# Kernel tuning notes

Measured on AMD Instinct MI355X. Metric: run time of the kernel, lower is better.

## Reference

```python
import jax, jax.numpy as jnp
import numpy as np

N = 50000   # num_nodes
T = 8       # num_time_steps
C = 64      # feature width (num_features == hidden == num_classes == 64, forced by the module's shape constraints)
E = 800000  # num_edges


def temporal_conv(x, edge_index, time_index, W, b, perturb=None):
    """Faithful TemporalAGNNConv.forward: per-timestep masked scatter-add of
    neighbor features, concat over T, linear + relu. Implemented as a single
    fused (t, dst)-bucketed segment reduce instead of T separate propagates.
    Note: self.lin is dead code in the original; self-loop addition in the
    original would crash (time_index length mismatch) so edges are used as-is.
    """
    src, dst = edge_index[0], edge_index[1]
    msgs = x[src]                                   # [E, C] gather
    seg = time_index * N + dst                      # combined (t, node) bucket
    agg = jax.ops.segment_sum(msgs, seg, num_segments=T * N)   # [T*N, C]
    cat = agg.reshape(T, N, C).transpose(1, 0, 2).reshape(N, T * C)  # [N, T*C]
    out = jax.nn.relu(cat @ W + b)                  # temporal_lin + relu
    if perturb is not None:
        out = out + perturb
    return out


def setup_inputs() -> dict:
    key = jax.random.key(0)
    ks = jax.random.split(key, 11)
    x = jax.random.normal(ks[0], (N, C), jnp.float32)
    edge_index = jax.random.randint(ks[1], (2, E), 0, N, dtype=jnp.int32)
    time_index = jax.random.randint(ks[2], (E,), 0, T, dtype=jnp.int32)
    s_t = 1.0 / np.sqrt(T * C).astype(np.float32)
    # temporal_lin weights stored as [in, out] (torch Linear transposed)
    Wt1 = jax.random.uniform(ks[3], (T * C, C), jnp.float32, -s_t, s_t)
    bt1 = jax.random.uniform(ks[4], (C,), jnp.float32, -s_t, s_t)
    Wt2 = jax.random.uniform(ks[5], (T * C, C), jnp.float32, -s_t, s_t)
    bt2 = jax.random.uniform(ks[6], (C,), jnp.float32, -s_t, s_t)
    s_a1 = 1.0 / np.sqrt(C).astype(np.float32)
    Wa1 = jax.random.uniform(ks[7], (C, 128), jnp.float32, -s_a1, s_a1)
    ba1 = jax.random.uniform(ks[8], (128,), jnp.float32, -s_a1, s_a1)
    s_a2 = 1.0 / np.sqrt(128).astype(np.float32)
    Wa2 = jax.random.uniform(ks[9], (128, C), jnp.float32, -s_a2, s_a2)
    ba2 = jax.random.uniform(ks[10], (C,), jnp.float32, -s_a2, s_a2)
    return {"x": x, "edge_index": edge_index, "time_index": time_index,
            "Wt1": Wt1, "bt1": bt1, "Wt2": Wt2, "bt2": bt2,
            "Wa1": Wa1, "ba1": ba1, "Wa2": Wa2, "ba2": ba2}


def reference(x, edge_index, time_index, Wt1, bt1, Wt2, bt2, Wa1, ba1, Wa2, ba2):
    h1 = jax.nn.relu(temporal_conv(x, edge_index, time_index, Wt1, bt1))   # conv1 + relu
    h2 = temporal_conv(h1, edge_index, time_index, Wt2, bt2)               # conv2 (output width C)
    adv = jax.nn.relu(h2 @ Wa1 + ba1) @ Wa2 + ba2                          # adversary MLP -> [N, C]
    out = temporal_conv(x, edge_index, time_index, Wt1, bt1, perturb=adv)  # conv1 again + perturbation
    return out
```

## Files before the change

### kernel.cpp

```cpp
#include <hip/hip_runtime.h>

#define N_NODES 50000
#define C_FEAT  64
#define E_EDGES 800000
#define KEYS    400000
#define NBLK1   391
#define DPB     16
#define NTILES  (N_NODES / DPB)
#define PBLK_X  1563
#define PBLK_W  128
#define PBLK_A  64
#define PBLK_H  391
#define DPART   6250
#define CONV_GRID 1024

typedef __attribute__((ext_vector_type(8))) short short8;
typedef __attribute__((ext_vector_type(4))) float f32x4;

__device__ __forceinline__ float bf2f(unsigned short u) {
    union { unsigned int i; float f; } v; v.i = ((unsigned int)u) << 16; return v.f;
}
__device__ __forceinline__ unsigned short f2bf(float f) {
    union { float f; unsigned int i; } v; v.f = f;
    unsigned int r = v.i + 0x7fff + ((v.i >> 16) & 1);
    return (unsigned short)(r >> 16);
}

__global__ __launch_bounds__(256) void prep_hist(const float* __restrict__ x,
                                                 const float* __restrict__ W1,
                                                 const float* __restrict__ W2,
                                                 const float* __restrict__ Wa1,
                                                 const float* __restrict__ Wa2,
                                                 const int* __restrict__ dst,
                                                 const int* __restrict__ tix,
                                                 unsigned short* __restrict__ xb,
                                                 unsigned short* __restrict__ WT1,
                                                 unsigned short* __restrict__ WT2,
                                                 unsigned short* __restrict__ Wa1T,
                                                 unsigned short* __restrict__ Wa2T,
                                                 int* __restrict__ cnt) {
    const int b = blockIdx.x;
    if (b < PBLK_X) {
        int base = (b * 256 + threadIdx.x) * 8;
        if (base < N_NODES * 64) {
            float4 a = *(const float4*)(x + base);
            float4 c = *(const float4*)(x + base + 4);
            short8 o;
            o[0] = (short)f2bf(a.x); o[1] = (short)f2bf(a.y);
            o[2] = (short)f2bf(a.z); o[3] = (short)f2bf(a.w);
            o[4] = (short)f2bf(c.x); o[5] = (short)f2bf(c.y);
            o[6] = (short)f2bf(c.z); o[7] = (short)f2bf(c.w);
            *(short8*)(xb + base) = o;
        }
    } else if (b < PBLK_X + PBLK_W) {
        int i = (b - PBLK_X) * 256 + threadIdx.x;
        int n = i >> 9, k = i & 511;
        WT1[i] = f2bf(W1[k * 64 + n]);
        WT2[i] = f2bf(W2[k * 64 + n]);
    } else if (b < PBLK_X + PBLK_W + PBLK_A) {
        int i = (b - PBLK_X - PBLK_W) * 256 + threadIdx.x;
        if (i < 8192) {
            int n = i >> 6, k = i & 63;
            Wa1T[i] = f2bf(Wa1[k * 128 + n]);
        } else {
            int ii = i - 8192;
            int n = ii >> 7, k = ii & 127;
            Wa2T[ii] = f2bf(Wa2[k * 64 + n]);
        }
    } else {
        int bb = b - PBLK_X - PBLK_W - PBLK_A;
        const int e0 = bb * 2048 + threadIdx.x * 8;
        if (e0 < E_EDGES) {
            int4 d0 = *(const int4*)(dst + e0);
            int4 d1 = *(const int4*)(dst + e0 + 4);
            int4 t0 = *(const int4*)(tix + e0);
            int4 t1 = *(const int4*)(tix + e0 + 4);
            int dd[8] = {d0.x, d0.y, d0.z, d0.w, d1.x, d1.y, d1.z, d1.w};
            int tt[8] = {t0.x, t0.y, t0.z, t0.w, t1.x, t1.y, t1.z, t1.w};
            #pragma unroll
            for (int k = 0; k < 8; ++k)
                atomicAdd(&cnt[dd[k] * 8 + tt[k]], 1);
        }
    }
}

__global__ __launch_bounds__(256) void scan_all(int* __restrict__ cnt,
                                                int* __restrict__ bsum,
                                                int* __restrict__ chunkoff,
                                                int* __restrict__ done) {
    __shared__ int wsum[4];
    __shared__ int ticket;
    const int tid = threadIdx.x;
    const int lane = tid & 63;
    const int wave = tid >> 6;
    const int i4 = blockIdx.x * 256 + tid;
    int4 v = make_int4(0, 0, 0, 0);
    const bool ok = (i4 * 4 < KEYS);
    if (ok) v = ((const int4*)cnt)[i4];
    int s = v.x + v.y + v.z + v.w;
    int sc = s;
    #pragma unroll
    for (int d = 1; d < 64; d <<= 1) {
        int o = __shfl_up(sc, d, 64);
        if (lane >= d) sc += o;
    }
    if (lane == 63) wsum[wave] = sc;
    __syncthreads();
    int wbase = 0;
    #pragma unroll
    for (int w = 0; w < 4; ++w) wbase += (w < wave) ? wsum[w] : 0;
    int base = wbase + sc - s;
    int4 o;
    o.x = base;
    o.y = base + v.x;
    o.z = o.y + v.y;
    o.w = o.z + v.z;
    if (ok) ((int4*)cnt)[i4] = o;
    if (tid == 255) {
        bsum[blockIdx.x] = wbase + sc;
        __threadfence();
        ticket = atomicAdd(done, 1);
    }
    __syncthreads();
    if (ticket == NBLK1 - 1 && wave == 0) {
        int carry = 0;
        #pragma unroll
        for (int g = 0; g < (NBLK1 + 63) / 64; ++g) {
            int j = g * 64 + lane;
            int val = (j < NBLK1) ? atomicAdd(&bsum[j], 0) : 0;
            int scn = val;
            #pragma unroll
            for (int d = 1; d < 64; d <<= 1) {
                int oo = __shfl_up(scn, d, 64);
                if (lane >= d) scn += oo;
            }
            if (j < NBLK1) chunkoff[j] = carry + scn - val;
            carry += __shfl(scn, 63, 64);
        }
    }
}

__global__ __launch_bounds__(256) void scatter_edges(const int* __restrict__ src,
                                                     const int* __restrict__ dst,
                                                     const int* __restrict__ tix,
                                                     int* __restrict__ cursor,
                                                     const int* __restrict__ chunkoff,
                                                     int* __restrict__ elist) {
    const int g = blockIdx.x & 7;
    const int lo = g * DPART;
    const int e0 = (blockIdx.x >> 3) * 2048 + threadIdx.x * 8;
    if (e0 < E_EDGES) {
        int4 d0 = *(const int4*)(dst + e0);
        int4 d1 = *(const int4*)(dst + e0 + 4);
        int4 t0 = *(const int4*)(tix + e0);
        int4 t1 = *(const int4*)(tix + e0 + 4);
        int4 s0 = *(const int4*)(src + e0);
        int4 s1 = *(const int4*)(src + e0 + 4);
        int dd[8] = {d0.x, d0.y, d0.z, d0.w, d1.x, d1.y, d1.z, d1.w};
        int tt[8] = {t0.x, t0.y, t0.z, t0.w, t1.x, t1.y, t1.z, t1.w};
        int ss[8] = {s0.x, s0.y, s0.z, s0.w, s1.x, s1.y, s1.z, s1.w};
        #pragma unroll
        for (int k = 0; k < 8; ++k) {
            if ((unsigned)(dd[k] - lo) < (unsigned)DPART) {
                int key = dd[k] * 8 + tt[k];
                int pos = chunkoff[key >> 10] + atomicAdd(&cursor[key], 1);
                elist[pos] = ss[k] | (tt[k] << 16) | ((dd[k] & 15) << 19);
            }
        }
    }
}

#define FLUSH(P, V)                                                                   \
    { int _k = (P) >> 16;                                                             \
      if (_k != cur) { scat[cur >> 3][(cur & 7) * 64 + c] = f2bf(acc);                \
                       acc = 0.f; cur = _k; }                                         \
      acc += (V); }

#define EDGE(K)                                                                       \
    int p##K = __builtin_amdgcn_readlane(pv, e + K);                                  \
    float v##K = bf2f(Xb[(size_t)(p##K & 0xffff) * 64 + c]);

template <bool ADV>
__global__ __launch_bounds__(512, 8) void fused_conv(const unsigned short* __restrict__ Xb,
                                                     const unsigned short* __restrict__ WT,
                                                     const float* __restrict__ bias,
                                                     const int* __restrict__ segend,
                                                     const int* __restrict__ chunkoff,
                                                     const int* __restrict__ elist,
                                                     unsigned short* __restrict__ Hb,
                                                     const unsigned short* __restrict__ Wa1T,
                                                     const float* __restrict__ ba1,
                                                     const unsigned short* __restrict__ Wa2T,
                                                     const float* __restrict__ ba2,
                                                     const unsigned short* __restrict__ h1r,
                                                     float* __restrict__ outF) {
    __shared__ __attribute__((aligned(16))) unsigned short scat[DPB][520];
    unsigned short (*sH)[72]  = (unsigned short(*)[72])&scat[0][0];
    unsigned short (*sT)[136] = (unsigned short(*)[136])((char*)scat + 4096);
    const int lane = threadIdx.x & 63;
    const int wave = threadIdx.x >> 6;
    const int c = lane;

    for (int tile = blockIdx.x; tile < NTILES; tile += CONV_GRID) {
        const int dbase = tile * DPB;

        {
            short8 z = {};
            *(short8*)&scat[wave * 2 + 0][lane * 8] = z;
            *(short8*)&scat[wave * 2 + 1][lane * 8] = z;
        }

        const int dpair = dbase + wave * 2;
        const int k0 = dpair * 8;
        const int sbeg = (dpair == 0) ? 0 : chunkoff[(k0 - 1) >> 10] + segend[k0 - 1];
        const int send = chunkoff[(k0 + 15) >> 10] + segend[k0 + 15];
        int pv = (lane < send - sbeg) ? elist[sbeg + lane] : 0;

        {
            int i = sbeg;
            int cur = 0;
            float acc = 0.f;
            if (i < send) cur = __builtin_amdgcn_readlane(pv, 0) >> 16;
            while (i < send) {
                int cnt = send - i; cnt = (cnt > 64) ? 64 : cnt;
                int pvn = 0;
                if (i + 64 < send) pvn = (lane < send - i - 64) ? elist[i + 64 + lane] : 0;
                int e = 0;
                for (; e + 15 < cnt; e += 16) {
                    EDGE(0)  EDGE(1)  EDGE(2)  EDGE(3)
                    EDGE(4)  EDGE(5)  EDGE(6)  EDGE(7)
                    EDGE(8)  EDGE(9)  EDGE(10) EDGE(11)
                    EDGE(12) EDGE(13) EDGE(14) EDGE(15)
                    FLUSH(p0, v0)   FLUSH(p1, v1)   FLUSH(p2, v2)   FLUSH(p3, v3)
                    FLUSH(p4, v4)   FLUSH(p5, v5)   FLUSH(p6, v6)   FLUSH(p7, v7)
                    FLUSH(p8, v8)   FLUSH(p9, v9)   FLUSH(p10, v10) FLUSH(p11, v11)
                    FLUSH(p12, v12) FLUSH(p13, v13) FLUSH(p14, v14) FLUSH(p15, v15)
                }
                if (e + 7 < cnt) {
                    EDGE(0) EDGE(1) EDGE(2) EDGE(3) EDGE(4) EDGE(5) EDGE(6) EDGE(7)
                    FLUSH(p0, v0) FLUSH(p1, v1) FLUSH(p2, v2) FLUSH(p3, v3)
                    FLUSH(p4, v4) FLUSH(p5, v5) FLUSH(p6, v6) FLUSH(p7, v7)
                    e += 8;
                }
                if (e + 3 < cnt) {
                    EDGE(0) EDGE(1) EDGE(2) EDGE(3)
                    FLUSH(p0, v0) FLUSH(p1, v1) FLUSH(p2, v2) FLUSH(p3, v3)
                    e += 4;
                }
                if (e + 1 < cnt) {
                    EDGE(0) EDGE(1)
                    FLUSH(p0, v0) FLUSH(p1, v1)
                    e += 2;
                }
                if (e < cnt) {
                    EDGE(0)
                    FLUSH(p0, v0)
                }
                i += 64;
                pv = pvn;
            }
            if (sbeg < send)
                scat[cur >> 3][(cur & 7) * 64 + c] = f2bf(acc);
        }
        __syncthreads();

        const int m = lane & 15;
        const int quad = lane >> 4;
        f32x4 acc4 = {0.f, 0.f, 0.f, 0.f};
        if (wave < 4) {
            const int n0 = wave * 16;
            const unsigned short* wrow = WT + (size_t)(n0 + m) * 512;
            #pragma unroll
            for (int kc = 0; kc < 16; ++kc) {
                short8 af = *(const short8*)&scat[m][kc * 32 + quad * 8];
                short8 bf = *(const short8*)(wrow + kc * 32 + quad * 8);
                acc4 = __builtin_amdgcn_mfma_f32_16x16x32_bf16(af, bf, acc4, 0, 0, 0);
            }
        }

        if (!ADV) {
            if (wave < 4) {
                const int col = wave * 16 + m;
                const float bcol = bias[col];
                #pragma unroll
                for (int r = 0; r < 4; ++r) {
                    int node = dbase + quad * 4 + r;
                    Hb[(size_t)node * 64 + col] = f2bf(fmaxf(acc4[r] + bcol, 0.f));
                }
            }
        } else {
            __syncthreads();
            if (wave < 4) {
                const int col = wave * 16 + m;
                const float bcol = bias[col];
                #pragma unroll
                for (int r = 0; r < 4; ++r)
                    sH[quad * 4 + r][col] = f2bf(fmaxf(acc4[r] + bcol, 0.f));
            }
            __syncthreads();
            {
                f32x4 a1 = {0.f, 0.f, 0.f, 0.f};
                const int col = wave * 16 + m;
                #pragma unroll
                for (int kc = 0; kc < 2; ++kc) {
                    short8 af = *(const short8*)&sH[m][kc * 32 + quad * 8];
                    short8 bf = *(const short8*)(Wa1T + (size_t)col * 64 + kc * 32 + quad * 8);
                    a1 = __builtin_amdgcn_mfma_f32_16x16x32_bf16(af, bf, a1, 0, 0, 0);
                }
                const float b1 = ba1[col];
                #pragma unroll
                for (int r = 0; r < 4; ++r)
                    sT[quad * 4 + r][col] = f2bf(fmaxf(a1[r] + b1, 0.f));
            }
            __syncthreads();
            if (wave < 4) {
                f32x4 a2 = {0.f, 0.f, 0.f, 0.f};
                const int col = wave * 16 + m;
                #pragma unroll
                for (int kc = 0; kc < 4; ++kc) {
                    short8 af = *(const short8*)&sT[m][kc * 32 + quad * 8];
                    short8 bf = *(const short8*)(Wa2T + (size_t)col * 128 + kc * 32 + quad * 8);
                    a2 = __builtin_amdgcn_mfma_f32_16x16x32_bf16(af, bf, a2, 0, 0, 0);
                }
                const float b2 = ba2[col];
                #pragma unroll
                for (int r = 0; r < 4; ++r) {
                    int node = dbase + quad * 4 + r;
                    outF[(size_t)node * 64 + col] =
                        a2[r] + b2 + bf2f(h1r[(size_t)node * 64 + col]);
                }
            }
        }
        __syncthreads();
    }
}

extern "C" void kernel_launch(void* const* d_in, const int* in_sizes, int n_in,
                              void* d_out, int out_size, void* d_ws, size_t ws_size,
                              hipStream_t stream) {
    const float* x   = (const float*)d_in[0];
    const int*   ei  = (const int*)d_in[1];
    const int*   tix = (const int*)d_in[2];
    const float* Wt1 = (const float*)d_in[3];
    const float* bt1 = (const float*)d_in[4];
    const float* Wt2 = (const float*)d_in[5];
    const float* bt2 = (const float*)d_in[6];
    const float* Wa1 = (const float*)d_in[7];
    const float* ba1 = (const float*)d_in[8];
    const float* Wa2 = (const float*)d_in[9];
    const float* ba2 = (const float*)d_in[10];
    float* out = (float*)d_out;

    const int* src = ei;
    const int* dst = ei + E_EDGES;

    unsigned short* xb   = (unsigned short*)d_ws;
    unsigned short* h1b  = xb + (size_t)N_NODES * 64;
    unsigned short* h2b  = h1b + (size_t)N_NODES * 64;
    unsigned short* WT1  = h2b + (size_t)N_NODES * 64;
    unsigned short* WT2  = WT1 + 64 * 512;
    unsigned short* Wa1T = WT2 + 64 * 512;
    unsigned short* Wa2T = Wa1T + 8192;
    int* cnt      = (int*)(Wa2T + 8192);
    int* bsum     = cnt + KEYS;
    int* chunkoff = bsum + 512;
    int* done     = chunkoff + 512;
    int* elist    = done + 64;

    hipMemsetAsync(cnt, 0, (KEYS + 512 + 512 + 64) * sizeof(int), stream);
    prep_hist<<<PBLK_X + PBLK_W + PBLK_A + PBLK_H, 256, 0, stream>>>(
        x, Wt1, Wt2, Wa1, Wa2, dst, tix, xb, WT1, WT2, Wa1T, Wa2T, cnt);
    scan_all<<<NBLK1, 256, 0, stream>>>(cnt, bsum, chunkoff, done);
    scatter_edges<<<8 * 391, 256, 0, stream>>>(src, dst, tix, cnt, chunkoff, elist);

    fused_conv<false><<<CONV_GRID, 512, 0, stream>>>(
        xb, WT1, bt1, cnt, chunkoff, elist, h1b,
        nullptr, nullptr, nullptr, nullptr, nullptr, nullptr);
    fused_conv<true><<<CONV_GRID, 512, 0, stream>>>(
        h1b, WT2, bt2, cnt, chunkoff, elist, nullptr,
        Wa1T, ba1, Wa2T, ba2, h1b, out);
}
```

Before: 274.6 us.

## Balance edge work across waves with fp32 LDS accumulation and boundary atomics

Instead of each wave handling the edges of a fixed pair of destination nodes, the tile's whole edge range is split evenly across the 8 waves. Partial sums that cross wave boundaries are merged with LDS float atomics on each wave's first and last segment. The scatter buffer becomes fp32 and is converted to bf16 when the MFMA operands are loaded. This is meant to remove load imbalance from skewed per-node degrees, at the cost of a doubled LDS footprint, an extra barrier and per-kc conversion work.

```diff
diff --git a/kernel.cpp b/kernel.cpp
--- a/kernel.cpp
+++ b/kernel.cpp
@@ -13,6 +13,7 @@
 #define PBLK_H  391
 #define DPART   6250
 #define CONV_GRID 1024
+#define RS      516
 
 typedef __attribute__((ext_vector_type(8))) short short8;
 typedef __attribute__((ext_vector_type(4))) float f32x4;
@@ -172,8 +173,10 @@
 
 #define FLUSH(P, V)                                                                   \
     { int _k = (P) >> 16;                                                             \
-      if (_k != cur) { scat[cur >> 3][(cur & 7) * 64 + c] = f2bf(acc);                \
-                       acc = 0.f; cur = _k; }                                         \
+      if (_k != cur) {                                                               \
+          float* sp = scatf + (cur >> 3) * RS + (cur & 7) * 64 + c;                   \
+          if (first) { atomicAdd(sp, acc); first = false; } else *sp = acc;           \
+          acc = 0.f; cur = _k; }                                                      \
       acc += (V); }
 
 #define EDGE(K)                                                                       \
@@ -194,37 +197,46 @@
                                                      const float* __restrict__ ba2,
                                                      const unsigned short* __restrict__ h1r,
                                                      float* __restrict__ outF) {
-    __shared__ __attribute__((aligned(16))) unsigned short scat[DPB][520];
-    unsigned short (*sH)[72]  = (unsigned short(*)[72])&scat[0][0];
-    unsigned short (*sT)[136] = (unsigned short(*)[136])((char*)scat + 4096);
+    __shared__ __attribute__((aligned(16))) float scatf[DPB * RS];
+    unsigned short (*sH)[72]  = (unsigned short(*)[72])scatf;
+    unsigned short (*sT)[136] = (unsigned short(*)[136])((char*)scatf + 4096);
     const int lane = threadIdx.x & 63;
     const int wave = threadIdx.x >> 6;
+    const int tid  = threadIdx.x;
     const int c = lane;
 
     for (int tile = blockIdx.x; tile < NTILES; tile += CONV_GRID) {
         const int dbase = tile * DPB;
 
         {
-            short8 z = {};
-            *(short8*)&scat[wave * 2 + 0][lane * 8] = z;
-            *(short8*)&scat[wave * 2 + 1][lane * 8] = z;
-        }
-
-        const int dpair = dbase + wave * 2;
-        const int k0 = dpair * 8;
-        const int sbeg = (dpair == 0) ? 0 : chunkoff[(k0 - 1) >> 10] + segend[k0 - 1];
-        const int send = chunkoff[(k0 + 15) >> 10] + segend[k0 + 15];
-        int pv = (lane < send - sbeg) ? elist[sbeg + lane] : 0;
-
-        {
-            int i = sbeg;
-            int cur = 0;
+            f32x4 z = {0.f, 0.f, 0.f, 0.f};
+            #pragma unroll
+            for (int j = tid; j < DPB * RS / 4; j += 512)
+                *(f32x4*)&scatf[j * 4] = z;
+        }
+
+        const int k0 = dbase * 8;
+        const int beg = (dbase == 0) ? 0 : chunkoff[(k0 - 1) >> 10] + segend[k0 - 1];
+        const int end = chunkoff[(k0 + 127) >> 10] + segend[k0 + 127];
+        const int cntE = end - beg;
+        const int pw = (cntE + 7) >> 3;
+        int wbeg = beg + wave * pw;
+        int wend = wbeg + pw;
+        if (wbeg > end) wbeg = end;
+        if (wend > end) wend = end;
+
+        __syncthreads();
+
+        if (wbeg < wend) {
+            int pv = (lane < wend - wbeg) ? elist[wbeg + lane] : 0;
+            int i = wbeg;
+            int cur = __builtin_amdgcn_readlane(pv, 0) >> 16;
             float acc = 0.f;
-            if (i < send) cur = __builtin_amdgcn_readlane(pv, 0) >> 16;
-            while (i < send) {
-                int cnt = send - i; cnt = (cnt > 64) ? 64 : cnt;
+            bool first = true;
+            while (i < wend) {
+                int cnt = wend - i; cnt = (cnt > 64) ? 64 : cnt;
                 int pvn = 0;
-                if (i + 64 < send) pvn = (lane < send - i - 64) ? elist[i + 64 + lane] : 0;
+                if (i + 64 < wend) pvn = (lane < wend - i - 64) ? elist[i + 64 + lane] : 0;
                 int e = 0;
                 for (; e + 15 < cnt; e += 16) {
                     EDGE(0)  EDGE(1)  EDGE(2)  EDGE(3)
@@ -259,8 +271,8 @@
                 i += 64;
                 pv = pvn;
             }
-            if (sbeg < send)
-                scat[cur >> 3][(cur & 7) * 64 + c] = f2bf(acc);
+            float* sp = scatf + (cur >> 3) * RS + (cur & 7) * 64 + c;
+            atomicAdd(sp, acc);
         }
         __syncthreads();
 
@@ -270,9 +282,16 @@
         if (wave < 4) {
             const int n0 = wave * 16;
             const unsigned short* wrow = WT + (size_t)(n0 + m) * 512;
+            const float* arow = scatf + m * RS;
             #pragma unroll
             for (int kc = 0; kc < 16; ++kc) {
-                short8 af = *(const short8*)&scat[m][kc * 32 + quad * 8];
+                f32x4 a0 = *(const f32x4*)(arow + kc * 32 + quad * 8);
+                f32x4 a1 = *(const f32x4*)(arow + kc * 32 + quad * 8 + 4);
+                short8 af;
+                af[0] = (short)f2bf(a0.x); af[1] = (short)f2bf(a0.y);
+                af[2] = (short)f2bf(a0.z); af[3] = (short)f2bf(a0.w);
+                af[4] = (short)f2bf(a1.x); af[5] = (short)f2bf(a1.y);
+                af[6] = (short)f2bf(a1.z); af[7] = (short)f2bf(a1.w);
                 short8 bf = *(const short8*)(wrow + kc * 32 + quad * 8);
                 acc4 = __builtin_amdgcn_mfma_f32_16x16x32_bf16(af, bf, acc4, 0, 0, 0);
             }
```

Result: slower. 288.3 us (+5.0%).
